# Optimization experiments

Measured on AMD Instinct MI355X. Metric: run time of the kernel, lower is better.

Reference implementation:

```python
import jax, jax.numpy as jnp
import numpy as np

B, I, H = 4096, 1024, 1024
LN_EPS = 1e-5


def setup_inputs() -> dict:
    key = jax.random.key(0)
    ks = jax.random.split(key, 7)
    s = 1.0 / np.sqrt(H)  # PyTorch LSTMCell init scale
    return {
        "input": jax.random.normal(ks[0], (B, I), jnp.float32),
        "h": jax.random.normal(ks[1], (B, H), jnp.float32),
        "c": jax.random.normal(ks[2], (B, H), jnp.float32),
        "w_ih": jax.random.normal(ks[3], (4 * H, I), jnp.float32) * s,
        "w_hh": jax.random.normal(ks[4], (4 * H, H), jnp.float32) * s,
        "b_ih": jax.random.normal(ks[5], (4 * H,), jnp.float32) * s,
        "b_hh": jax.random.normal(ks[6], (4 * H,), jnp.float32) * s,
        "ln_gamma": jnp.ones((4 * H,), jnp.float32),
        "ln_beta": jnp.zeros((4 * H,), jnp.float32),
    }


def reference(input, h, c, w_ih, w_hh, b_ih, b_hh, ln_gamma, ln_beta):
    # gates: [B, 4H] = x @ W_ih^T + h @ W_hh^T + biases
    gates = (jnp.einsum("bi,gi->bg", input, w_ih)
             + jnp.einsum("bh,gh->bg", h, w_hh)
             + b_ih + b_hh)
    # LayerNorm over the 4H gate axis
    mu = jnp.mean(gates, axis=-1, keepdims=True)
    var = jnp.mean(jnp.square(gates - mu), axis=-1, keepdims=True)
    gates = (gates - mu) * jax.lax.rsqrt(var + LN_EPS) * ln_gamma + ln_beta
    # PyTorch gate order: input, forget, cell(g), output
    i_g, f_g, g_g, o_g = jnp.split(gates, 4, axis=-1)
    new_c = jax.nn.sigmoid(f_g) * c + jax.nn.sigmoid(i_g) * jnp.tanh(g_g)
    new_h = jax.nn.sigmoid(o_g) * jnp.tanh(new_c)
    return (new_h, new_c)
```

## Files before the change

kernel.cpp:

```cpp
#include <hip/hip_runtime.h>
#include <hip/hip_bf16.h>
#include <stdint.h>

#define LN_EPS 1e-5f

typedef __attribute__((ext_vector_type(8))) short bf16x8;
typedef __attribute__((ext_vector_type(4))) float f32x4;
typedef __attribute__((ext_vector_type(4))) short short4v;

__device__ __forceinline__ short f2bf(float x) {
    union { __hip_bfloat16 b; short s; } u;
    u.b = __float2bfloat16(x);
    return u.s;
}

__device__ __forceinline__ float sigm(float x) { return 1.f / (1.f + __expf(-x)); }
__device__ __forceinline__ float tanh_f(float x) {
    x = fminf(15.f, fmaxf(-15.f, x));
    float e = __expf(2.f * x);
    return (e - 1.f) / (e + 1.f);
}

__global__ __launch_bounds__(256)
void pack_cat_bf16(const float* __restrict__ s0, const float* __restrict__ s1,
                   short* __restrict__ dst, int rows)
{
    const long total4 = (long)rows * 2048 / 4;
    for (long q = blockIdx.x * (long)blockDim.x + threadIdx.x; q < total4;
         q += (long)gridDim.x * blockDim.x) {
        long n = q << 2;
        long r = n >> 11;
        int  k = (int)(n & 2047);
        const float* src = (k < 1024) ? (s0 + (r << 10) + k)
                                      : (s1 + (r << 10) + (k - 1024));
        float4 v = *(const float4*)src;
        short4v o;
        o.x = f2bf(v.x); o.y = f2bf(v.y); o.z = f2bf(v.z); o.w = f2bf(v.w);
        *(short4v*)(dst + n) = o;
    }
}

#define BM 128
#define BN 128
#define BKK 32

__global__ __launch_bounds__(256)
void gemm_bt_bf16(const short* __restrict__ A, const short* __restrict__ B,
                  float* __restrict__ C, int M, int N, int K)
{
    __shared__ short sA[BM * BKK];
    __shared__ short sB[BN * BKK];
    const int t    = threadIdx.x;
    const int lane = t & 63;
    const int wave = t >> 6;
    const int wr   = wave >> 1;
    const int wc   = wave & 1;
    const int brow = blockIdx.y * BM;
    const int bcol = blockIdx.x * BN;

    const int r4 = t >> 2;
    const int k8 = (t & 3) << 3;

    const short* Ag = A + (long)(brow + r4) * K + k8;
    const short* Bg = B + (long)(bcol + r4) * K + k8;

    auto sA3 = (__attribute__((address_space(3))) char*)sA;
    auto sB3 = (__attribute__((address_space(3))) char*)sB;
    const int ldsOff = wave * 1024;

    f32x4 acc[4][4] = {};

    const short* sAr = sA + (wr * 64 + (lane & 15)) * BKK + ((lane >> 4) << 3);
    const short* sBr = sB + (wc * 64 + (lane & 15)) * BKK + ((lane >> 4) << 3);

    for (int kt = 0; kt < K; kt += BKK) {
        __syncthreads();
        __builtin_amdgcn_global_load_lds(
            (const __attribute__((address_space(1))) void*)(Ag + kt),
            (__attribute__((address_space(3))) void*)(sA3 + ldsOff), 16, 0, 0);
        __builtin_amdgcn_global_load_lds(
            (const __attribute__((address_space(1))) void*)(Ag + kt + 64 * K),
            (__attribute__((address_space(3))) void*)(sA3 + 4096 + ldsOff), 16, 0, 0);
        __builtin_amdgcn_global_load_lds(
            (const __attribute__((address_space(1))) void*)(Bg + kt),
            (__attribute__((address_space(3))) void*)(sB3 + ldsOff), 16, 0, 0);
        __builtin_amdgcn_global_load_lds(
            (const __attribute__((address_space(1))) void*)(Bg + kt + 64 * K),
            (__attribute__((address_space(3))) void*)(sB3 + 4096 + ldsOff), 16, 0, 0);
        __syncthreads();

        bf16x8 af[4], bfr[4];
        #pragma unroll
        for (int m = 0; m < 4; ++m) af[m]  = *(const bf16x8*)(sAr + m * 16 * BKK);
        #pragma unroll
        for (int n = 0; n < 4; ++n) bfr[n] = *(const bf16x8*)(sBr + n * 16 * BKK);

        #pragma unroll
        for (int m = 0; m < 4; ++m)
            #pragma unroll
            for (int n = 0; n < 4; ++n)
                acc[m][n] = __builtin_amdgcn_mfma_f32_16x16x32_bf16(
                    af[m], bfr[n], acc[m][n], 0, 0, 0);
    }

    const int row0 = brow + wr * 64 + ((lane >> 4) << 2);
    const int col0 = bcol + wc * 64 + (lane & 15);
    #pragma unroll
    for (int m = 0; m < 4; ++m)
        #pragma unroll
        for (int n = 0; n < 4; ++n) {
            float* Cp = C + (long)(row0 + m * 16) * N + col0 + n * 16;
            #pragma unroll
            for (int j = 0; j < 4; ++j)
                Cp[(long)j * N] = acc[m][n][j];
        }
}

__global__ __launch_bounds__(256)
void ln_act_kernel(const float* __restrict__ gates,
                   const float* __restrict__ b_ih, const float* __restrict__ b_hh,
                   const float* __restrict__ gamma, const float* __restrict__ beta,
                   const float* __restrict__ c,
                   float* __restrict__ out_h, float* __restrict__ out_c)
{
    __shared__ float sg[4096];
    __shared__ float rs[4], rq[4];
    const int b = blockIdx.x;
    const int t = threadIdx.x;
    const float4* grow = (const float4*)(gates + ((long)b << 12));
    const float4* bi4  = (const float4*)b_ih;
    const float4* bh4  = (const float4*)b_hh;

    float sum = 0.f, sq = 0.f;
    #pragma unroll
    for (int j = 0; j < 4; ++j) {
        int idx = t + j * 256;
        float4 v  = grow[idx];
        float4 bi = bi4[idx];
        float4 bh = bh4[idx];
        v.x += bi.x + bh.x;  v.y += bi.y + bh.y;
        v.z += bi.z + bh.z;  v.w += bi.w + bh.w;
        ((float4*)sg)[idx] = v;
        sum += v.x + v.y + v.z + v.w;
        sq  += v.x * v.x + v.y * v.y + v.z * v.z + v.w * v.w;
    }
    #pragma unroll
    for (int off = 32; off > 0; off >>= 1) {
        sum += __shfl_down(sum, off);
        sq  += __shfl_down(sq, off);
    }
    if ((t & 63) == 0) { rs[t >> 6] = sum; rq[t >> 6] = sq; }
    __syncthreads();
    sum = rs[0] + rs[1] + rs[2] + rs[3];
    sq  = rq[0] + rq[1] + rq[2] + rq[3];
    const float mu   = sum * (1.f / 4096.f);
    const float rstd = rsqrtf(sq * (1.f / 4096.f) - mu * mu + LN_EPS);

    #pragma unroll
    for (int j = 0; j < 4; ++j) {
        int hc = t + j * 256;
        float iv = (sg[hc]        - mu) * rstd * gamma[hc]        + beta[hc];
        float fv = (sg[1024 + hc] - mu) * rstd * gamma[1024 + hc] + beta[1024 + hc];
        float gv = (sg[2048 + hc] - mu) * rstd * gamma[2048 + hc] + beta[2048 + hc];
        float ov = (sg[3072 + hc] - mu) * rstd * gamma[3072 + hc] + beta[3072 + hc];
        float cc = c[((long)b << 10) + hc];
        float nc = sigm(fv) * cc + sigm(iv) * tanh_f(gv);
        float nh = sigm(ov) * tanh_f(nc);
        out_h[((long)b << 10) + hc] = nh;
        out_c[((long)b << 10) + hc] = nc;
    }
}

extern "C" void kernel_launch(void* const* d_in, const int* in_sizes, int n_in,
                              void* d_out, int out_size, void* d_ws, size_t ws_size,
                              hipStream_t stream)
{
    const float* x    = (const float*)d_in[0];
    const float* h    = (const float*)d_in[1];
    const float* c    = (const float*)d_in[2];
    const float* w_ih = (const float*)d_in[3];
    const float* w_hh = (const float*)d_in[4];
    const float* b_ih = (const float*)d_in[5];
    const float* b_hh = (const float*)d_in[6];
    const float* gam  = (const float*)d_in[7];
    const float* bet  = (const float*)d_in[8];
    float* out = (float*)d_out;
    (void)in_sizes; (void)n_in; (void)out_size; (void)ws_size;

    const int B = 4096, H = 1024;
    const int K = 2048;
    const int G = 4096;

    char*  ws    = (char*)d_ws;
    short* Acat  = (short*)ws;
    short* Wcat  = (short*)(ws + (size_t)16 * 1024 * 1024);
    float* gates = (float*)(ws + (size_t)32 * 1024 * 1024);

    pack_cat_bf16<<<1024, 256, 0, stream>>>(x, h, Acat, B);
    pack_cat_bf16<<<1024, 256, 0, stream>>>(w_ih, w_hh, Wcat, G);

    dim3 grid(G / BN, B / BM);
    gemm_bt_bf16<<<grid, 256, 0, stream>>>(Acat, Wcat, gates, B, G, K);

    ln_act_kernel<<<B, 256, 0, stream>>>(gates, b_ih, b_hh, gam, bet, c,
                                         out, out + (size_t)B * H);
}
```

Before: 262.4 us.

## Replace GEMM with 256x256 double-buffered swizzled-LDS pipelined kernel; vectorize LN epilogue

Replaces the 128x128 single-buffered bf16 GEMM with a 256x256-tile, 512-thread kernel. It uses a 64-wide K step, XOR-swizzled LDS layout and double-buffered asynchronous global-to-LDS staging, interleaved across four MFMA phases with explicit waitcnt, barriers and setprio. The goal is to hide load latency, cut LDS bank conflicts and raise data reuse per tile, at the cost of 128KB LDS per block and a grid of only 256 blocks. The LN/activation epilogue is also changed to use float4 loads and stores.

```diff
diff --git a/kernel.cpp b/kernel.cpp
--- a/kernel.cpp
+++ b/kernel.cpp
@@ -13,7 +13,6 @@
     u.b = __float2bfloat16(x);
     return u.s;
 }
-
 __device__ __forceinline__ float sigm(float x) { return 1.f / (1.f + __expf(-x)); }
 __device__ __forceinline__ float tanh_f(float x) {
     x = fminf(15.f, fmaxf(-15.f, x));
@@ -40,79 +39,170 @@
     }
 }
 
-#define BM 128
-#define BN 128
-#define BKK 32
-
-__global__ __launch_bounds__(256)
-void gemm_bt_bf16(const short* __restrict__ A, const short* __restrict__ B,
-                  float* __restrict__ C, int M, int N, int K)
-{
-    __shared__ short sA[BM * BKK];
-    __shared__ short sB[BN * BKK];
-    const int t    = threadIdx.x;
-    const int lane = t & 63;
-    const int wave = t >> 6;
-    const int wr   = wave >> 1;
-    const int wc   = wave & 1;
-    const int brow = blockIdx.y * BM;
-    const int bcol = blockIdx.x * BN;
-
-    const int r4 = t >> 2;
-    const int k8 = (t & 3) << 3;
-
-    const short* Ag = A + (long)(brow + r4) * K + k8;
-    const short* Bg = B + (long)(bcol + r4) * K + k8;
-
-    auto sA3 = (__attribute__((address_space(3))) char*)sA;
-    auto sB3 = (__attribute__((address_space(3))) char*)sB;
-    const int ldsOff = wave * 1024;
-
-    f32x4 acc[4][4] = {};
-
-    const short* sAr = sA + (wr * 64 + (lane & 15)) * BKK + ((lane >> 4) << 3);
-    const short* sBr = sB + (wc * 64 + (lane & 15)) * BKK + ((lane >> 4) << 3);
-
-    for (int kt = 0; kt < K; kt += BKK) {
-        __syncthreads();
+#define SWZ(x) ((x) ^ ((((x) >> 9) & 1) << 5))
+
+__device__ __forceinline__ void stage_half(const short* __restrict__ G, int rowBase,
+                                           int t, char* halfRegion, int tid)
+{
+    #pragma unroll
+    for (int j = 0; j < 2; ++j) {
+        const int p   = j * 8192 + tid * 16;
+        const int l   = SWZ(p);
+        const int row = l >> 7;
+        const int kel = (l & 127) >> 1;
+        const short* src = G + (size_t)(rowBase + row) * 2048 + t * 64 + kel;
         __builtin_amdgcn_global_load_lds(
-            (const __attribute__((address_space(1))) void*)(Ag + kt),
-            (__attribute__((address_space(3))) void*)(sA3 + ldsOff), 16, 0, 0);
-        __builtin_amdgcn_global_load_lds(
-            (const __attribute__((address_space(1))) void*)(Ag + kt + 64 * K),
-            (__attribute__((address_space(3))) void*)(sA3 + 4096 + ldsOff), 16, 0, 0);
-        __builtin_amdgcn_global_load_lds(
-            (const __attribute__((address_space(1))) void*)(Bg + kt),
-            (__attribute__((address_space(3))) void*)(sB3 + ldsOff), 16, 0, 0);
-        __builtin_amdgcn_global_load_lds(
-            (const __attribute__((address_space(1))) void*)(Bg + kt + 64 * K),
-            (__attribute__((address_space(3))) void*)(sB3 + 4096 + ldsOff), 16, 0, 0);
-        __syncthreads();
-
-        bf16x8 af[4], bfr[4];
+            (const __attribute__((address_space(1))) void*)src,
+            (__attribute__((address_space(3))) void*)(halfRegion + j * 8192 + ((tid >> 6) << 10)),
+            16, 0, 0);
+    }
+}
+
+__device__ __forceinline__ bf16x8 ldsRead(const char* region, int logical)
+{
+    return *(const bf16x8*)(region + SWZ(logical));
+}
+
+#define BARR()      __builtin_amdgcn_s_barrier()
+#define WAIT_LGKM() do { asm volatile("s_waitcnt lgkmcnt(0)" ::: "memory"); \
+                         __builtin_amdgcn_sched_barrier(0); } while (0)
+#define WAIT_VM6()  asm volatile("s_waitcnt vmcnt(6)" ::: "memory")
+#define WAIT_VM0()  asm volatile("s_waitcnt vmcnt(0)" ::: "memory")
+#define MFMA16(a, b, c) __builtin_amdgcn_mfma_f32_16x16x32_bf16((a), (b), (c), 0, 0, 0)
+
+__global__ __launch_bounds__(512, 2)
+void gemm256_8p(const short* __restrict__ A, const short* __restrict__ B,
+                float* __restrict__ C)
+{
+    __shared__ __align__(1024) char smem[131072];
+    const int tid  = threadIdx.x;
+    const int lane = tid & 63;
+    const int wave = tid >> 6;
+    const int wr = wave >> 2;
+    const int wc = wave & 3;
+    const int bx = blockIdx.x & 15, by = blockIdx.x >> 4;
+    const int brow = by * 256, bcol = bx * 256;
+    const int NT = 32;
+
+    const int aBase = (wr * 128 + (lane & 15)) * 128 + ((lane >> 4) << 4);
+    const int bBase = (wc * 64  + (lane & 15)) * 128 + ((lane >> 4) << 4);
+
+    f32x4 acc[8][4] = {};
+    bf16x8 aF[4][2], bF[2][2][2];
+
+    char* Areg0 = smem;             char* Breg0 = smem + 32768;
+    char* Areg1 = smem + 65536;     char* Breg1 = smem + 65536 + 32768;
+
+    stage_half(A, brow +   0, 0, Areg0 +     0, tid);
+    stage_half(A, brow + 128, 0, Areg0 + 16384, tid);
+    stage_half(B, bcol +   0, 0, Breg0 +     0, tid);
+    stage_half(B, bcol + 128, 0, Breg0 + 16384, tid);
+    stage_half(B, bcol +   0, 1, Breg1 +     0, tid);
+    stage_half(B, bcol + 128, 1, Breg1 + 16384, tid);
+    stage_half(A, brow +   0, 1, Areg1 +     0, tid);
+    WAIT_VM6();
+    BARR();
+
+    for (int it = 0; it < 16; ++it) {
+        const int t0 = it * 2;
         #pragma unroll
-        for (int m = 0; m < 4; ++m) af[m]  = *(const bf16x8*)(sAr + m * 16 * BKK);
-        #pragma unroll
-        for (int n = 0; n < 4; ++n) bfr[n] = *(const bf16x8*)(sBr + n * 16 * BKK);
-
-        #pragma unroll
-        for (int m = 0; m < 4; ++m)
-            #pragma unroll
-            for (int n = 0; n < 4; ++n)
-                acc[m][n] = __builtin_amdgcn_mfma_f32_16x16x32_bf16(
-                    af[m], bfr[n], acc[m][n], 0, 0, 0);
-    }
-
-    const int row0 = brow + wr * 64 + ((lane >> 4) << 2);
+        for (int hb = 0; hb < 2; ++hb) {
+            const int t = t0 + hb;
+            const char* Ar = hb ? Areg1 : Areg0;
+            const char* Br = hb ? Breg1 : Breg0;
+            char* ArN = hb ? Areg0 : Areg1;
+            char* AwC = hb ? Areg1 : Areg0;
+            char* BwC = hb ? Breg1 : Breg0;
+
+            #pragma unroll
+            for (int m = 0; m < 4; ++m)
+                #pragma unroll
+                for (int ks = 0; ks < 2; ++ks)
+                    aF[m][ks] = ldsRead(Ar, aBase + m * 2048 + ks * 64);
+            #pragma unroll
+            for (int n = 0; n < 2; ++n)
+                #pragma unroll
+                for (int ks = 0; ks < 2; ++ks)
+                    bF[0][n][ks] = ldsRead(Br, bBase + n * 2048 + ks * 64);
+            if (t + 1 < NT) stage_half(A, brow + 128, t + 1, ArN + 16384, tid);
+            BARR(); WAIT_LGKM();
+            __builtin_amdgcn_s_setprio(1);
+            #pragma unroll
+            for (int m = 0; m < 4; ++m)
+                #pragma unroll
+                for (int n = 0; n < 2; ++n)
+                    #pragma unroll
+                    for (int ks = 0; ks < 2; ++ks)
+                        acc[m][n] = MFMA16(aF[m][ks], bF[0][n][ks], acc[m][n]);
+            __builtin_amdgcn_s_setprio(0);
+            BARR();
+
+            #pragma unroll
+            for (int n = 0; n < 2; ++n)
+                #pragma unroll
+                for (int ks = 0; ks < 2; ++ks)
+                    bF[1][n][ks] = ldsRead(Br, bBase + (2 + n) * 2048 + ks * 64);
+            BARR(); WAIT_LGKM();
+            __builtin_amdgcn_s_setprio(1);
+            #pragma unroll
+            for (int m = 0; m < 4; ++m)
+                #pragma unroll
+                for (int n = 0; n < 2; ++n)
+                    #pragma unroll
+                    for (int ks = 0; ks < 2; ++ks)
+                        acc[m][2 + n] = MFMA16(aF[m][ks], bF[1][n][ks], acc[m][2 + n]);
+            __builtin_amdgcn_s_setprio(0);
+            BARR();
+
+            #pragma unroll
+            for (int m = 0; m < 4; ++m)
+                #pragma unroll
+                for (int ks = 0; ks < 2; ++ks)
+                    aF[m][ks] = ldsRead(Ar, aBase + (4 + m) * 2048 + ks * 64);
+            if (t + 2 < NT) stage_half(B, bcol + 0, t + 2, BwC + 0, tid);
+            BARR(); WAIT_LGKM();
+            __builtin_amdgcn_s_setprio(1);
+            #pragma unroll
+            for (int m = 0; m < 4; ++m)
+                #pragma unroll
+                for (int n = 0; n < 2; ++n)
+                    #pragma unroll
+                    for (int ks = 0; ks < 2; ++ks)
+                        acc[4 + m][2 + n] = MFMA16(aF[m][ks], bF[1][n][ks], acc[4 + m][2 + n]);
+            __builtin_amdgcn_s_setprio(0);
+            BARR();
+
+            if (t + 2 < NT) {
+                stage_half(B, bcol + 128, t + 2, BwC + 16384, tid);
+                stage_half(A, brow +   0, t + 2, AwC +     0, tid);
+                WAIT_VM6();
+            } else {
+                WAIT_VM0();
+            }
+            BARR(); WAIT_LGKM();
+            __builtin_amdgcn_s_setprio(1);
+            #pragma unroll
+            for (int m = 0; m < 4; ++m)
+                #pragma unroll
+                for (int n = 0; n < 2; ++n)
+                    #pragma unroll
+                    for (int ks = 0; ks < 2; ++ks)
+                        acc[4 + m][n] = MFMA16(aF[m][ks], bF[0][n][ks], acc[4 + m][n]);
+            __builtin_amdgcn_s_setprio(0);
+            BARR();
+        }
+    }
+
+    const int row0 = brow + wr * 128 + ((lane >> 4) << 2);
     const int col0 = bcol + wc * 64 + (lane & 15);
     #pragma unroll
-    for (int m = 0; m < 4; ++m)
+    for (int m = 0; m < 8; ++m)
         #pragma unroll
         for (int n = 0; n < 4; ++n) {
-            float* Cp = C + (long)(row0 + m * 16) * N + col0 + n * 16;
+            float* Cp = C + (size_t)(row0 + m * 16) * 4096 + col0 + n * 16;
             #pragma unroll
             for (int j = 0; j < 4; ++j)
-                Cp[(long)j * N] = acc[m][n][j];
+                Cp[(size_t)j * 4096] = acc[m][n][j];
         }
 }
 
@@ -156,19 +246,29 @@
     const float mu   = sum * (1.f / 4096.f);
     const float rstd = rsqrtf(sq * (1.f / 4096.f) - mu * mu + LN_EPS);
 
-    #pragma unroll
-    for (int j = 0; j < 4; ++j) {
-        int hc = t + j * 256;
-        float iv = (sg[hc]        - mu) * rstd * gamma[hc]        + beta[hc];
-        float fv = (sg[1024 + hc] - mu) * rstd * gamma[1024 + hc] + beta[1024 + hc];
-        float gv = (sg[2048 + hc] - mu) * rstd * gamma[2048 + hc] + beta[2048 + hc];
-        float ov = (sg[3072 + hc] - mu) * rstd * gamma[3072 + hc] + beta[3072 + hc];
-        float cc = c[((long)b << 10) + hc];
-        float nc = sigm(fv) * cc + sigm(iv) * tanh_f(gv);
-        float nh = sigm(ov) * tanh_f(nc);
-        out_h[((long)b << 10) + hc] = nh;
-        out_c[((long)b << 10) + hc] = nc;
-    }
+    const float4* sg4 = (const float4*)sg;
+    const float4* gm4 = (const float4*)gamma;
+    const float4* bt4 = (const float4*)beta;
+    float4 vi = sg4[t],        vf = sg4[256 + t];
+    float4 vg = sg4[512 + t],  vo = sg4[768 + t];
+    float4 gi = gm4[t], gf = gm4[256 + t], gg = gm4[512 + t], go = gm4[768 + t];
+    float4 zi = bt4[t], zf = bt4[256 + t], zg = bt4[512 + t], zo = bt4[768 + t];
+    float4 cc = ((const float4*)c)[((long)b << 8) + t];
+    float4 nh, nc;
+    {
+        float i0, f0, g0, o0;
+        #define DO_COMP(X)                                                    \
+            i0 = (vi.X - mu) * rstd * gi.X + zi.X;                            \
+            f0 = (vf.X - mu) * rstd * gf.X + zf.X;                            \
+            g0 = (vg.X - mu) * rstd * gg.X + zg.X;                            \
+            o0 = (vo.X - mu) * rstd * go.X + zo.X;                            \
+            nc.X = sigm(f0) * cc.X + sigm(i0) * tanh_f(g0);                   \
+            nh.X = sigm(o0) * tanh_f(nc.X);
+        DO_COMP(x) DO_COMP(y) DO_COMP(z) DO_COMP(w)
+        #undef DO_COMP
+    }
+    ((float4*)out_h)[((long)b << 8) + t] = nh;
+    ((float4*)out_c)[((long)b << 8) + t] = nc;
 }
 
 extern "C" void kernel_launch(void* const* d_in, const int* in_sizes, int n_in,
@@ -187,9 +287,7 @@
     float* out = (float*)d_out;
     (void)in_sizes; (void)n_in; (void)out_size; (void)ws_size;
 
-    const int B = 4096, H = 1024;
-    const int K = 2048;
-    const int G = 4096;
+    const int B = 4096, H = 1024, G = 4096;
 
     char*  ws    = (char*)d_ws;
     short* Acat  = (short*)ws;
@@ -199,8 +297,7 @@
     pack_cat_bf16<<<1024, 256, 0, stream>>>(x, h, Acat, B);
     pack_cat_bf16<<<1024, 256, 0, stream>>>(w_ih, w_hh, Wcat, G);
 
-    dim3 grid(G / BN, B / BM);
-    gemm_bt_bf16<<<grid, 256, 0, stream>>>(Acat, Wcat, gates, B, G, K);
+    gemm256_8p<<<dim3(256), dim3(512), 0, stream>>>(Acat, Wcat, gates);
 
     ln_act_kernel<<<B, 256, 0, stream>>>(gates, b_ih, b_hh, gam, bet, c,
                                          out, out + (size_t)B * H);
```

Result: faster. 233.4 us (-11.1%).
